# Kernel optimization log

Measured on AMD Instinct MI355X. Metric: run time of the kernel, lower is better.

The kernel has to match this reference:

```python
import jax, jax.numpy as jnp
import numpy as np
from jax import lax

N_NODES = 100000
N_EDGES = 1600000
NUM_GRAPHS = 2000
F_IN = 64
HIDDEN = 64
NUM_LAYERS = 3
K = 7
NUM_CLASSES = 10


def setup_inputs() -> dict:
    key = jax.random.key(0)
    ks = jax.random.split(key, 16)
    x = jax.random.normal(ks[0], (N_NODES, F_IN), jnp.float32)
    edge_index = jax.random.randint(ks[1], (2, N_EDGES), 0, N_NODES)
    batch = jnp.sort(jax.random.randint(ks[2], (N_NODES,), 0, NUM_GRAPHS))
    s = 1.0 / np.sqrt(HIDDEN)
    p = lambda k_, sh: jax.random.uniform(k_, sh, jnp.float32, -s, s)
    return dict(
        x=x, edge_index=edge_index, batch=batch,
        W1l=p(ks[3], (F_IN, HIDDEN)), b1=p(ks[4], (HIDDEN,)), W1r=p(ks[5], (F_IN, HIDDEN)),
        W2l=p(ks[6], (HIDDEN, HIDDEN)), b2=p(ks[7], (HIDDEN,)), W2r=p(ks[8], (HIDDEN, HIDDEN)),
        W3l=p(ks[9], (HIDDEN, HIDDEN)), b3=p(ks[10], (HIDDEN,)), W3r=p(ks[11], (HIDDEN, HIDDEN)),
        conv1d_w=p(ks[12], (32, HIDDEN, NUM_LAYERS)), conv1d_b=jnp.zeros((32,), jnp.float32),
        lin1_w=p(ks[13], (32 * (K - NUM_LAYERS + 1), HIDDEN)), lin1_b=jnp.zeros((HIDDEN,), jnp.float32),
        lin2_w=p(ks[14], (HIDDEN, NUM_CLASSES)), lin2_b=jnp.zeros((NUM_CLASSES,), jnp.float32),
    )


def _sage(x, src, dst, Wl, b, Wr):
    # PyG SAGEConv (aggr='mean'): lin_l(mean_j x_j) + lin_r(x_i); lin_l carries the bias.
    n = x.shape[0]
    msum = jax.ops.segment_sum(x[src], dst, num_segments=n)          # [N, D] gather+scatter
    cnt = jax.ops.segment_sum(jnp.ones((src.shape[0],), x.dtype), dst, num_segments=n)
    mean = msum / jnp.maximum(cnt, 1.0)[:, None]
    return mean @ Wl + b + x @ Wr


def _sort_pool(x, batch, num_graphs, k):
    # SortAggregation: per graph, sort nodes descending by last feature channel,
    # keep top-k, zero-pad short graphs, flatten to [B, k*D].
    N, D = x.shape
    perm = jnp.lexsort((-x[:, -1], batch))  # primary: graph id, secondary: desc last channel
    sb = batch[perm]
    counts = jax.ops.segment_sum(jnp.ones((N,), jnp.int32), batch, num_segments=num_graphs)
    starts = jnp.concatenate([jnp.zeros((1,), jnp.int32), jnp.cumsum(counts)[:-1]])
    rank = jnp.arange(N, dtype=jnp.int32) - starts[sb]
    valid = rank < k
    b_idx = jnp.where(valid, sb, num_graphs)  # route overflow nodes to dummy row
    r_idx = jnp.where(valid, rank, 0)
    out = jnp.zeros((num_graphs + 1, k, D), x.dtype).at[b_idx, r_idx].set(x[perm])
    return out[:num_graphs].reshape(num_graphs, k * D)


def reference(x, edge_index, batch, W1l, b1, W1r, W2l, b2, W2r, W3l, b3, W3r,
              conv1d_w, conv1d_b, lin1_w, lin1_b, lin2_w, lin2_b):
    src, dst = edge_index[0], edge_index[1]
    h = jax.nn.relu(_sage(x, src, dst, W1l, b1, W1r))
    h = jax.nn.relu(_sage(h, src, dst, W2l, b2, W2r))
    h = jax.nn.relu(_sage(h, src, dst, W3l, b3, W3r))
    g = _sort_pool(h, batch, NUM_GRAPHS, K)                       # [B, K*H]
    g = g.reshape(NUM_GRAPHS, K, HIDDEN).transpose(0, 2, 1)       # [B, H, K]
    c = lax.conv_general_dilated(g, conv1d_w, (1,), 'VALID',
                                 dimension_numbers=('NCH', 'OIH', 'NCH'))
    c = jax.nn.relu(c + conv1d_b[None, :, None])                  # [B, 32, K-ks+1]
    flat = c.reshape(NUM_GRAPHS, -1)
    h1 = jax.nn.relu(flat @ lin1_w + lin1_b)                      # dropout = identity (eval)
    logits = h1 @ lin2_w + lin2_b
    return jax.nn.log_softmax(logits, axis=-1)
```

## Files before the change

kernel.cpp:

```cpp
#include <hip/hip_runtime.h>
#include <hip/hip_bf16.h>

#define NN 100000
#define NE 1600000
#define NG 2000
#define KTOP 7

#define BNODES 128
#define NBKT 782
#define EPB 8192
#define NL1B 196
#define L2CAP 4096

#define GEMM_BLOCKS 768
#define SMEM_FLOATS (64 * 68 + 2 * 64 * 64)

#define FMA4C(av, B, acc) do { \
    acc[0] = fmaf(av, B.x, acc[0]); acc[1] = fmaf(av, B.y, acc[1]); \
    acc[2] = fmaf(av, B.z, acc[2]); acc[3] = fmaf(av, B.w, acc[3]); } while (0)

__device__ __forceinline__ void gemm_body(int bid, int nblocks, float* smem,
        const float* __restrict__ X, const float* __restrict__ Wl,
        const float* __restrict__ Wr, const float* __restrict__ bias,
        float* __restrict__ XL, float* __restrict__ T, int n) {
    float* As = smem;
    float* Bl = smem + 64 * 68;
    float* Br = Bl + 64 * 64;
    int t = threadIdx.x;

    #pragma unroll
    for (int q = 0; q < 4; ++q) {
        int idx = t + q * 256;
        ((float4*)Bl)[idx] = ((const float4*)Wl)[idx];
        ((float4*)Br)[idx] = ((const float4*)Wr)[idx];
    }
    int ty4 = (t >> 4) * 4, tx4 = (t & 15) * 4;
    float b0 = bias[tx4 + 0], b1v = bias[tx4 + 1], b2v = bias[tx4 + 2], b3v = bias[tx4 + 3];
    int ntiles = (n + 63) / 64;
    for (int tile = bid; tile < ntiles; tile += nblocks) {
        int n0 = tile * 64;
        #pragma unroll
        for (int q = 0; q < 4; ++q) {
            int f = t + q * 256;
            int node = f >> 4, seg = f & 15;
            int g = n0 + node;
            float4 v = make_float4(0.f, 0.f, 0.f, 0.f);
            if (g < n) v = *(const float4*)&X[(size_t)g * 64 + seg * 4];
            *(float4*)&As[node * 68 + seg * 4] = v;
        }
        __syncthreads();
        float accl[4][4] = {{0.f}}, accr[4][4] = {{0.f}};
        for (int kc = 0; kc < 64; kc += 4) {
            float4 Av[4], L[4], R[4];
            #pragma unroll
            for (int i = 0; i < 4; ++i) Av[i] = *(const float4*)&As[(ty4 + i) * 68 + kc];
            #pragma unroll
            for (int j = 0; j < 4; ++j) {
                L[j] = *(const float4*)&Bl[(kc + j) * 64 + tx4];
                R[j] = *(const float4*)&Br[(kc + j) * 64 + tx4];
            }
            #pragma unroll
            for (int i = 0; i < 4; ++i) {
                FMA4C(Av[i].x, L[0], accl[i]); FMA4C(Av[i].y, L[1], accl[i]);
                FMA4C(Av[i].z, L[2], accl[i]); FMA4C(Av[i].w, L[3], accl[i]);
                FMA4C(Av[i].x, R[0], accr[i]); FMA4C(Av[i].y, R[1], accr[i]);
                FMA4C(Av[i].z, R[2], accr[i]); FMA4C(Av[i].w, R[3], accr[i]);
            }
        }
        #pragma unroll
        for (int i = 0; i < 4; ++i) {
            int g = n0 + ty4 + i;
            if (g < n) {
                *(float4*)&XL[(size_t)g * 64 + tx4] =
                    make_float4(accl[i][0], accl[i][1], accl[i][2], accl[i][3]);
                *(float4*)&T[(size_t)g * 64 + tx4] =
                    make_float4(accr[i][0] + b0, accr[i][1] + b1v, accr[i][2] + b2v, accr[i][3] + b3v);
            }
        }
        __syncthreads();
    }
}

__global__ __launch_bounds__(256) void k_gemm(const float* __restrict__ X,
        const float* __restrict__ Wl, const float* __restrict__ Wr,
        const float* __restrict__ bias,
        float* __restrict__ XL, float* __restrict__ T, int n) {
    __shared__ float smem[SMEM_FLOATS];
    gemm_body(blockIdx.x, GEMM_BLOCKS, smem, X, Wl, Wr, bias, XL, T, n);
}

__global__ __launch_bounds__(256) void k_front(const float* __restrict__ X,
        const float* __restrict__ Wl, const float* __restrict__ Wr,
        const float* __restrict__ bias, float* __restrict__ XL, float* __restrict__ T,
        const int* __restrict__ edst, int* __restrict__ bh,
        const int* __restrict__ bat, int* __restrict__ gstart) {
    __shared__ float smem[SMEM_FLOATS];
    int bid = blockIdx.x, t = threadIdx.x;
    if (bid < GEMM_BLOCKS) {
        gemm_body(bid, GEMM_BLOCKS, smem, X, Wl, Wr, bias, XL, T, NN);
    } else if (bid < GEMM_BLOCKS + NL1B) {
        int bk = bid - GEMM_BLOCKS;
        int* h = (int*)smem;
        for (int q = t; q < NBKT; q += 256) h[q] = 0;
        __syncthreads();
        int e0 = bk * EPB, e1 = min(e0 + EPB, NE);
        for (int e = e0 + t; e < e1; e += 256) atomicAdd(&h[edst[e] >> 7], 1);
        __syncthreads();
        for (int q = t; q < NBKT; q += 256) bh[bk * NBKT + q] = h[q];
    } else {
        int g = (bid - GEMM_BLOCKS - NL1B) * 256 + t;
        if (g <= NG) {
            int lo = 0, hi = NN;
            while (lo < hi) { int mid = (lo + hi) >> 1; if (bat[mid] < g) lo = mid + 1; else hi = mid; }
            gstart[g] = lo;
        }
    }
}

__global__ void k_colscan(int* __restrict__ bh, int* __restrict__ btot) {
    __shared__ int carry;
    int b = blockIdx.x, t = threadIdx.x;
    if (t == 0) carry = 0;
    __syncthreads();
    for (int base = 0; base < NL1B; base += 64) {
        int idx = base + t;
        int v = (idx < NL1B) ? bh[idx * NBKT + b] : 0;
        int x = v;
        #pragma unroll
        for (int off = 1; off < 64; off <<= 1) {
            int y = __shfl_up(x, off);
            if (t >= off) x += y;
        }
        int c = carry;
        if (idx < NL1B) bh[idx * NBKT + b] = c + x - v;
        __syncthreads();
        if (t == 63) carry = c + x;
        __syncthreads();
    }
    if (t == 0) btot[b] = carry;
}

__global__ void k_btscan(const int* __restrict__ btot, int* __restrict__ bstart) {
    __shared__ int s[1024];
    int t = threadIdx.x;
    int v = (t < NBKT) ? btot[t] : 0;
    s[t] = v; __syncthreads();
    for (int off = 1; off < 1024; off <<= 1) {
        int y = (t >= off) ? s[t - off] : 0;
        __syncthreads();
        s[t] += y;
        __syncthreads();
    }
    if (t < NBKT) bstart[t] = s[t] - v;
    if (t == NBKT - 1) bstart[NBKT] = s[t];
}

__global__ __launch_bounds__(256) void k_bscatter(const int* __restrict__ esrc,
        const int* __restrict__ edst, const int* __restrict__ bh,
        const int* __restrict__ bstart, int* __restrict__ ebuf) {
    __shared__ int cur[NBKT];
    int t = threadIdx.x, bk = blockIdx.x;
    for (int q = t; q < NBKT; q += 256) cur[q] = bstart[q] + bh[bk * NBKT + q];
    __syncthreads();
    int e0 = bk * EPB, e1 = min(e0 + EPB, NE);
    for (int e = e0 + t; e < e1; e += 256) {
        int d = edst[e], s = esrc[e];
        int pos = atomicAdd(&cur[d >> 7], 1);
        ebuf[pos] = s | ((d & 127) << 20);
    }
}

__global__ __launch_bounds__(128) void k_bbuild(const int* __restrict__ ebuf,
        const int* __restrict__ bstart, int* __restrict__ ce, int* __restrict__ ptr) {
    __shared__ int lord[L2CAP];
    __shared__ int cnt[BNODES], sc[BNODES], cursor[BNODES];
    int b = blockIdx.x, t = threadIdx.x;
    int base = bstart[b], nb = bstart[b + 1] - base;
    cnt[t] = 0;
    __syncthreads();
    for (int j = t; j < nb; j += 128) atomicAdd(&cnt[ebuf[base + j] >> 20], 1);
    __syncthreads();
    int v = cnt[t]; sc[t] = v; __syncthreads();
    for (int off = 1; off < 128; off <<= 1) {
        int y = (t >= off) ? sc[t - off] : 0;
        __syncthreads();
        sc[t] += y;
        __syncthreads();
    }
    int segend = sc[t], segstart = sc[t] - v;
    cursor[t] = segstart;
    __syncthreads();
    bool fits = (nb <= L2CAP);
    for (int j = t; j < nb; j += 128) {
        int pv = ebuf[base + j];
        int node = pv >> 20;
        int pos = atomicAdd(&cursor[node], 1);
        if (fits) lord[pos] = pv & 0xFFFFF;
        else ce[base + pos] = pv & 0xFFFFF;
    }
    __syncthreads();
    if (fits) {
        for (int a = segstart + 1; a < segend; ++a) {
            int val = lord[a]; int j = a - 1;
            while (j >= segstart && lord[j] > val) { lord[j + 1] = lord[j]; --j; }
            lord[j + 1] = val;
        }
        __syncthreads();
        for (int j = t; j < nb; j += 128) ce[base + j] = lord[j];
    } else {
        for (int a = segstart + 1; a < segend; ++a) {
            int val = ce[base + a]; int j = a - 1;
            while (j >= segstart && ce[base + j] > val) { ce[base + j + 1] = ce[base + j]; --j; }
            ce[base + j + 1] = val;
        }
    }
    int node = b * BNODES + t;
    if (node <= NN) ptr[node] = base + segstart;
}

__global__ __launch_bounds__(256) void k_aggregate(const float* __restrict__ XL,
        float* __restrict__ Hout, const int* __restrict__ ptr, const int* __restrict__ ce,
        int n, float* __restrict__ key) {
    int wave = threadIdx.x >> 6, lane = threadIdx.x & 63;
    int i = blockIdx.x * 4 + wave;
    if (i >= n) return;
    int s = ptr[i], e = ptr[i + 1];
    int g = lane >> 4;
    int c4 = (lane & 15) * 4;
    float4 tv = *(const float4*)&Hout[(size_t)i * 64 + c4];
    float4 acc = make_float4(0.f, 0.f, 0.f, 0.f);
    int a = s;
    for (; a + 16 <= e; a += 16) {
        int r0 = ce[a + g], r1 = ce[a + 4 + g], r2 = ce[a + 8 + g], r3 = ce[a + 12 + g];
        float4 v0 = *(const float4*)&XL[(size_t)r0 * 64 + c4];
        float4 v1 = *(const float4*)&XL[(size_t)r1 * 64 + c4];
        float4 v2 = *(const float4*)&XL[(size_t)r2 * 64 + c4];
        float4 v3 = *(const float4*)&XL[(size_t)r3 * 64 + c4];
        acc.x += (v0.x + v1.x) + (v2.x + v3.x);
        acc.y += (v0.y + v1.y) + (v2.y + v3.y);
        acc.z += (v0.z + v1.z) + (v2.z + v3.z);
        acc.w += (v0.w + v1.w) + (v2.w + v3.w);
    }
    for (; a + 4 <= e; a += 4) {
        int r0 = ce[a + g];
        float4 v0 = *(const float4*)&XL[(size_t)r0 * 64 + c4];
        acc.x += v0.x; acc.y += v0.y; acc.z += v0.z; acc.w += v0.w;
    }
    if (g < e - a) {
        int r0 = ce[a + g];
        float4 v0 = *(const float4*)&XL[(size_t)r0 * 64 + c4];
        acc.x += v0.x; acc.y += v0.y; acc.z += v0.z; acc.w += v0.w;
    }
    #pragma unroll
    for (int off = 16; off < 64; off <<= 1) {
        acc.x += __shfl_xor(acc.x, off);
        acc.y += __shfl_xor(acc.y, off);
        acc.z += __shfl_xor(acc.z, off);
        acc.w += __shfl_xor(acc.w, off);
    }
    if (g == 0) {
        float cm = fmaxf((float)(e - s), 1.f);
        float4 h;
        h.x = fmaxf(acc.x / cm + tv.x, 0.f);
        h.y = fmaxf(acc.y / cm + tv.y, 0.f);
        h.z = fmaxf(acc.z / cm + tv.z, 0.f);
        h.w = fmaxf(acc.w / cm + tv.w, 0.f);
        *(float4*)&Hout[(size_t)i * 64 + c4] = h;
        if (key && (lane & 15) == 15) key[i] = h.w;
    }
}

__global__ __launch_bounds__(256) void k_topk(const float* __restrict__ key,
        const int* __restrict__ gstart, int* __restrict__ idx7, int G) {
    int wv = threadIdx.x >> 6, lane = threadIdx.x & 63;
    int b = blockIdx.x * 4 + wv;
    if (b >= G) return;
    int s = gstart[b], e = gstart[b + 1];
    float pk = 3.4e38f; int pi = -1;
    for (int r = 0; r < KTOP; ++r) {
        float bk = -1.f; int bi = -1;
        for (int i = s + lane; i < e; i += 64) {
            float k = key[i];
            bool elig = (k < pk) || (k == pk && i > pi);
            if (elig && (k > bk || (k == bk && (unsigned)i < (unsigned)bi))) { bk = k; bi = i; }
        }
        #pragma unroll
        for (int off = 1; off < 64; off <<= 1) {
            float ok = __shfl_xor(bk, off);
            int   oi = __shfl_xor(bi, off);
            if (ok > bk || (ok == bk && (unsigned)oi < (unsigned)bi)) { bk = ok; bi = oi; }
        }
        if (lane == 0) idx7[b * KTOP + r] = bi;
        pk = bk; pi = bi;
    }
}

__global__ __launch_bounds__(256) void k_head(const float* __restrict__ h3,
        const int* __restrict__ idx7,
        const float* __restrict__ cw, const float* __restrict__ cb,
        const float* __restrict__ l1w, const float* __restrict__ l1b,
        const float* __restrict__ l2w, const float* __restrict__ l2b,
        float* __restrict__ out, int G) {
    __shared__ float sw[32 * 64 * 3];
    __shared__ float s2w[64 * 10];
    __shared__ float sg[4][KTOP][64];
    __shared__ float sflat[4][160];
    __shared__ float sh1[4][64];
    __shared__ float slog[4][10];
    int t = threadIdx.x;
    for (int q = t; q < 32 * 64 * 3; q += 256) sw[q] = cw[q];
    for (int q = t; q < 640; q += 256) s2w[q] = l2w[q];
    int wv = t >> 6, lane = t & 63;
    int b = blockIdx.x * 4 + wv;
    for (int r = 0; r < KTOP; ++r) {
        int idx = idx7[b * KTOP + r];
        sg[wv][r][lane] = (idx >= 0) ? h3[(size_t)idx * 64 + lane] : 0.f;
    }
    __syncthreads();
    for (int idx = lane; idx < 160; idx += 64) {
        int o = idx / 5, p = idx % 5;
        float acc = cb[o];
        #pragma unroll
        for (int dt = 0; dt < 3; ++dt) {
            const float* wrow = &sw[(o * 64) * 3 + dt];
            const float* grow = &sg[wv][p + dt][0];
            for (int i = 0; i < 64; ++i) acc = fmaf(wrow[i * 3], grow[i], acc);
        }
        sflat[wv][idx] = fmaxf(acc, 0.f);
    }
    __syncthreads();
    {
        float acc = l1b[lane];
        for (int k = 0; k < 160; ++k) acc = fmaf(sflat[wv][k], l1w[k * 64 + lane], acc);
        sh1[wv][lane] = fmaxf(acc, 0.f);
    }
    __syncthreads();
    if (lane < 10) {
        float acc = l2b[lane];
        for (int k = 0; k < 64; ++k) acc = fmaf(sh1[wv][k], s2w[k * 10 + lane], acc);
        slog[wv][lane] = acc;
    }
    __syncthreads();
    if (lane < 10) {
        float m = -3.4e38f;
        for (int j = 0; j < 10; ++j) m = fmaxf(m, slog[wv][j]);
        float ssum = 0.f;
        for (int j = 0; j < 10; ++j) ssum += expf(slog[wv][j] - m);
        out[b * 10 + lane] = slog[wv][lane] - m - logf(ssum);
    }
}

extern "C" void kernel_launch(void* const* d_in, const int* in_sizes, int n_in,
                              void* d_out, int out_size, void* d_ws, size_t ws_size,
                              hipStream_t stream) {
    const float* x   = (const float*)d_in[0];
    const int*   ei  = (const int*)d_in[1];
    const int*   bat = (const int*)d_in[2];
    const float* W1l = (const float*)d_in[3], *b1 = (const float*)d_in[4], *W1r = (const float*)d_in[5];
    const float* W2l = (const float*)d_in[6], *b2 = (const float*)d_in[7], *W2r = (const float*)d_in[8];
    const float* W3l = (const float*)d_in[9], *b3 = (const float*)d_in[10], *W3r = (const float*)d_in[11];
    const float* cw  = (const float*)d_in[12], *cb  = (const float*)d_in[13];
    const float* l1w = (const float*)d_in[14], *l1b = (const float*)d_in[15];
    const float* l2w = (const float*)d_in[16], *l2b = (const float*)d_in[17];
    float* out = (float*)d_out;
    const int* esrc = ei;
    const int* edst = ei + NE;

    char* w = (char*)d_ws;
    size_t off = 0;
    auto take = [&](size_t bytes) { void* p = w + off; off = (off + bytes + 255) & ~(size_t)255; return p; };
    int*   bh      = (int*)take((size_t)NL1B * NBKT * 4);
    int*   btot    = (int*)take((size_t)NBKT * 4);
    int*   bstart  = (int*)take((size_t)(NBKT + 1) * 4);
    int*   gstart  = (int*)take((size_t)(NG + 1) * 4);
    int*   idx7    = (int*)take((size_t)NG * KTOP * 4);
    int*   ebuf    = (int*)take((size_t)NE * 4);
    int*   csr_ptr = (int*)take((size_t)(NN + 1) * 4);
    int*   csr_e   = (int*)take((size_t)NE * 4);
    float* XL      = (float*)take((size_t)NN * 64 * 4);
    float* Ha      = (float*)take((size_t)NN * 64 * 4);
    float* Hb      = (float*)take((size_t)NN * 64 * 4);
    float* key     = (float*)take((size_t)NN * 4);

    k_front<<<GEMM_BLOCKS + NL1B + 8, 256, 0, stream>>>(x, W1l, W1r, b1, XL, Ha,
                                                        edst, bh, bat, gstart);
    k_colscan<<<NBKT, 64, 0, stream>>>(bh, btot);
    k_btscan <<<1, 1024, 0, stream>>>(btot, bstart);
    k_bscatter<<<NL1B, 256, 0, stream>>>(esrc, edst, bh, bstart, ebuf);
    k_bbuild <<<NBKT, 128, 0, stream>>>(ebuf, bstart, csr_e, csr_ptr);

    k_aggregate<<<(NN + 3) / 4, 256, 0, stream>>>(XL, Ha, csr_ptr, csr_e, NN, nullptr);
    k_gemm<<<GEMM_BLOCKS, 256, 0, stream>>>(Ha, W2l, W2r, b2, XL, Hb, NN);
    k_aggregate<<<(NN + 3) / 4, 256, 0, stream>>>(XL, Hb, csr_ptr, csr_e, NN, nullptr);
    k_gemm<<<GEMM_BLOCKS, 256, 0, stream>>>(Hb, W3l, W3r, b3, XL, Ha, NN);
    k_aggregate<<<(NN + 3) / 4, 256, 0, stream>>>(XL, Ha, csr_ptr, csr_e, NN, key);

    k_topk<<<(NG + 3) / 4, 256, 0, stream>>>(key, gstart, idx7, NG);
    k_head<<<NG / 4, 256, 0, stream>>>(Ha, idx7, cw, cb, l1w, l1b, l2w, l2b, out, NG);
}
```

Baseline: 375.8 us.

## Fuse neighbor aggregation into next-layer GEMM and merge top-k into head

Each layer's mean aggregation and ReLU are now computed straight into the shared-memory A tile of the next layer's dual GEMM, so the hidden activation is never written to or re-read from global memory. The aggregation mapping also changes from one wave per node (16 lanes per float4 column group, with shuffle reductions) to four threads per node, each accumulating 16 contiguous features. The top-k selection is folded into the head kernel, and the idx7 buffer plus two launches are removed. The trade-off is less memory-level parallelism per node in the gather and fewer edges in flight per wave, which could hurt latency hiding. T is updated in place within a tile, and each tile reads its own T rows before any thread writes them.

```diff
diff --git a/kernel.cpp b/kernel.cpp
--- a/kernel.cpp
+++ b/kernel.cpp
@@ -13,31 +13,89 @@
 #define L2CAP 4096
 
 #define GEMM_BLOCKS 768
+#define NTILES 1563
 #define SMEM_FLOATS (64 * 68 + 2 * 64 * 64)
+
+#define ACC4(A, V) do { A.x += V.x; A.y += V.y; A.z += V.z; A.w += V.w; } while (0)
+#define ACC4P(A, U, W) do { A.x += U.x + W.x; A.y += U.y + W.y; \
+                            A.z += U.z + W.z; A.w += U.w + W.w; } while (0)
+
+__device__ __forceinline__ void agg_node(const float* __restrict__ XLp, const int* __restrict__ ce,
+        int s, int e, int fo, float4& a0, float4& a1, float4& a2, float4& a3) {
+    int a = s;
+    for (; a + 2 <= e; a += 2) {
+        const float4* p0 = (const float4*)(XLp + ((size_t)ce[a] << 6) + fo);
+        const float4* p1 = (const float4*)(XLp + ((size_t)ce[a + 1] << 6) + fo);
+        float4 u0 = p0[0], u1 = p0[1], u2 = p0[2], u3 = p0[3];
+        float4 w0 = p1[0], w1 = p1[1], w2 = p1[2], w3 = p1[3];
+        ACC4P(a0, u0, w0); ACC4P(a1, u1, w1); ACC4P(a2, u2, w2); ACC4P(a3, u3, w3);
+    }
+    if (a < e) {
+        const float4* p0 = (const float4*)(XLp + ((size_t)ce[a] << 6) + fo);
+        float4 u0 = p0[0], u1 = p0[1], u2 = p0[2], u3 = p0[3];
+        ACC4(a0, u0); ACC4(a1, u1); ACC4(a2, u2); ACC4(a3, u3);
+    }
+}
 
 #define FMA4C(av, B, acc) do { \
     acc[0] = fmaf(av, B.x, acc[0]); acc[1] = fmaf(av, B.y, acc[1]); \
     acc[2] = fmaf(av, B.z, acc[2]); acc[3] = fmaf(av, B.w, acc[3]); } while (0)
 
-__device__ __forceinline__ void gemm_body(int bid, int nblocks, float* smem,
-        const float* __restrict__ X, const float* __restrict__ Wl,
-        const float* __restrict__ Wr, const float* __restrict__ bias,
-        float* __restrict__ XL, float* __restrict__ T, int n) {
-    float* As = smem;
-    float* Bl = smem + 64 * 68;
-    float* Br = Bl + 64 * 64;
-    int t = threadIdx.x;
-
+__device__ __forceinline__ void gemm_tile(float* As, float* Bl, float* Br,
+        int n0, int ty4, int tx4, float b0, float b1v, float b2v, float b3v,
+        float* __restrict__ XL, float* __restrict__ T) {
+    float accl[4][4] = {{0.f}}, accr[4][4] = {{0.f}};
+    for (int kc = 0; kc < 64; kc += 4) {
+        float4 Av[4], L[4], R[4];
+        #pragma unroll
+        for (int i = 0; i < 4; ++i) Av[i] = *(const float4*)&As[(ty4 + i) * 68 + kc];
+        #pragma unroll
+        for (int j = 0; j < 4; ++j) {
+            L[j] = *(const float4*)&Bl[(kc + j) * 64 + tx4];
+            R[j] = *(const float4*)&Br[(kc + j) * 64 + tx4];
+        }
+        #pragma unroll
+        for (int i = 0; i < 4; ++i) {
+            FMA4C(Av[i].x, L[0], accl[i]); FMA4C(Av[i].y, L[1], accl[i]);
+            FMA4C(Av[i].z, L[2], accl[i]); FMA4C(Av[i].w, L[3], accl[i]);
+            FMA4C(Av[i].x, R[0], accr[i]); FMA4C(Av[i].y, R[1], accr[i]);
+            FMA4C(Av[i].z, R[2], accr[i]); FMA4C(Av[i].w, R[3], accr[i]);
+        }
+    }
+    #pragma unroll
+    for (int i = 0; i < 4; ++i) {
+        int g = n0 + ty4 + i;
+        if (g < NN) {
+            *(float4*)&XL[(size_t)g * 64 + tx4] =
+                make_float4(accl[i][0], accl[i][1], accl[i][2], accl[i][3]);
+            *(float4*)&T[(size_t)g * 64 + tx4] =
+                make_float4(accr[i][0] + b0, accr[i][1] + b1v, accr[i][2] + b2v, accr[i][3] + b3v);
+        }
+    }
+}
+
+__device__ __forceinline__ void stage_weights(float* Bl, float* Br,
+        const float* __restrict__ Wl, const float* __restrict__ Wr, int t) {
     #pragma unroll
     for (int q = 0; q < 4; ++q) {
         int idx = t + q * 256;
         ((float4*)Bl)[idx] = ((const float4*)Wl)[idx];
         ((float4*)Br)[idx] = ((const float4*)Wr)[idx];
     }
+}
+
+__device__ __forceinline__ void gemm_body(int bid, int nblocks, float* smem,
+        const float* __restrict__ X, const float* __restrict__ Wl,
+        const float* __restrict__ Wr, const float* __restrict__ bias,
+        float* __restrict__ XL, float* __restrict__ T) {
+    float* As = smem;
+    float* Bl = smem + 64 * 68;
+    float* Br = Bl + 64 * 64;
+    int t = threadIdx.x;
+    stage_weights(Bl, Br, Wl, Wr, t);
     int ty4 = (t >> 4) * 4, tx4 = (t & 15) * 4;
     float b0 = bias[tx4 + 0], b1v = bias[tx4 + 1], b2v = bias[tx4 + 2], b3v = bias[tx4 + 3];
-    int ntiles = (n + 63) / 64;
-    for (int tile = bid; tile < ntiles; tile += nblocks) {
+    for (int tile = bid; tile < NTILES; tile += nblocks) {
         int n0 = tile * 64;
         #pragma unroll
         for (int q = 0; q < 4; ++q) {
@@ -45,48 +103,80 @@
             int node = f >> 4, seg = f & 15;
             int g = n0 + node;
             float4 v = make_float4(0.f, 0.f, 0.f, 0.f);
-            if (g < n) v = *(const float4*)&X[(size_t)g * 64 + seg * 4];
+            if (g < NN) v = *(const float4*)&X[(size_t)g * 64 + seg * 4];
             *(float4*)&As[node * 68 + seg * 4] = v;
         }
         __syncthreads();
-        float accl[4][4] = {{0.f}}, accr[4][4] = {{0.f}};
-        for (int kc = 0; kc < 64; kc += 4) {
-            float4 Av[4], L[4], R[4];
-            #pragma unroll
-            for (int i = 0; i < 4; ++i) Av[i] = *(const float4*)&As[(ty4 + i) * 68 + kc];
-            #pragma unroll
-            for (int j = 0; j < 4; ++j) {
-                L[j] = *(const float4*)&Bl[(kc + j) * 64 + tx4];
-                R[j] = *(const float4*)&Br[(kc + j) * 64 + tx4];
-            }
-            #pragma unroll
-            for (int i = 0; i < 4; ++i) {
-                FMA4C(Av[i].x, L[0], accl[i]); FMA4C(Av[i].y, L[1], accl[i]);
-                FMA4C(Av[i].z, L[2], accl[i]); FMA4C(Av[i].w, L[3], accl[i]);
-                FMA4C(Av[i].x, R[0], accr[i]); FMA4C(Av[i].y, R[1], accr[i]);
-                FMA4C(Av[i].z, R[2], accr[i]); FMA4C(Av[i].w, R[3], accr[i]);
-            }
-        }
-        #pragma unroll
-        for (int i = 0; i < 4; ++i) {
-            int g = n0 + ty4 + i;
-            if (g < n) {
-                *(float4*)&XL[(size_t)g * 64 + tx4] =
-                    make_float4(accl[i][0], accl[i][1], accl[i][2], accl[i][3]);
-                *(float4*)&T[(size_t)g * 64 + tx4] =
-                    make_float4(accr[i][0] + b0, accr[i][1] + b1v, accr[i][2] + b2v, accr[i][3] + b3v);
-            }
-        }
-        __syncthreads();
-    }
-}
-
-__global__ __launch_bounds__(256) void k_gemm(const float* __restrict__ X,
+        gemm_tile(As, Bl, Br, n0, ty4, tx4, b0, b1v, b2v, b3v, XL, T);
+        __syncthreads();
+    }
+}
+
+__global__ __launch_bounds__(256) void k_aggemm(const float* __restrict__ XL_in,
+        float* __restrict__ T, const int* __restrict__ ptr, const int* __restrict__ ce,
         const float* __restrict__ Wl, const float* __restrict__ Wr,
-        const float* __restrict__ bias,
-        float* __restrict__ XL, float* __restrict__ T, int n) {
+        const float* __restrict__ bias, float* __restrict__ XL_out) {
     __shared__ float smem[SMEM_FLOATS];
-    gemm_body(blockIdx.x, GEMM_BLOCKS, smem, X, Wl, Wr, bias, XL, T, n);
+    float* As = smem;
+    float* Bl = smem + 64 * 68;
+    float* Br = Bl + 64 * 64;
+    int t = threadIdx.x;
+    stage_weights(Bl, Br, Wl, Wr, t);
+    int node_l = t >> 2;
+    int fo = (t & 3) * 16;
+    int ty4 = (t >> 4) * 4, tx4 = (t & 15) * 4;
+    float b0 = bias[tx4 + 0], b1v = bias[tx4 + 1], b2v = bias[tx4 + 2], b3v = bias[tx4 + 3];
+    for (int tile = blockIdx.x; tile < NTILES; tile += GEMM_BLOCKS) {
+        int n0 = tile * 64;
+        int i = n0 + node_l;
+        float4 h0 = make_float4(0.f, 0.f, 0.f, 0.f), h1 = h0, h2 = h0, h3 = h0;
+        if (i < NN) {
+            int s = ptr[i], e = ptr[i + 1];
+            agg_node(XL_in, ce, s, e, fo, h0, h1, h2, h3);
+            float inv = 1.f / fmaxf((float)(e - s), 1.f);
+            const float4* tp = (const float4*)(T + ((size_t)i << 6) + fo);
+            float4 t0 = tp[0], t1 = tp[1], t2 = tp[2], t3 = tp[3];
+            h0.x = fmaxf(h0.x * inv + t0.x, 0.f); h0.y = fmaxf(h0.y * inv + t0.y, 0.f);
+            h0.z = fmaxf(h0.z * inv + t0.z, 0.f); h0.w = fmaxf(h0.w * inv + t0.w, 0.f);
+            h1.x = fmaxf(h1.x * inv + t1.x, 0.f); h1.y = fmaxf(h1.y * inv + t1.y, 0.f);
+            h1.z = fmaxf(h1.z * inv + t1.z, 0.f); h1.w = fmaxf(h1.w * inv + t1.w, 0.f);
+            h2.x = fmaxf(h2.x * inv + t2.x, 0.f); h2.y = fmaxf(h2.y * inv + t2.y, 0.f);
+            h2.z = fmaxf(h2.z * inv + t2.z, 0.f); h2.w = fmaxf(h2.w * inv + t2.w, 0.f);
+            h3.x = fmaxf(h3.x * inv + t3.x, 0.f); h3.y = fmaxf(h3.y * inv + t3.y, 0.f);
+            h3.z = fmaxf(h3.z * inv + t3.z, 0.f); h3.w = fmaxf(h3.w * inv + t3.w, 0.f);
+        }
+        float* dst = &As[node_l * 68 + fo];
+        ((float4*)dst)[0] = h0; ((float4*)dst)[1] = h1;
+        ((float4*)dst)[2] = h2; ((float4*)dst)[3] = h3;
+        __syncthreads();
+        gemm_tile(As, Bl, Br, n0, ty4, tx4, b0, b1v, b2v, b3v, XL_out, T);
+        __syncthreads();
+    }
+}
+
+__global__ __launch_bounds__(256) void k_agg3(const float* __restrict__ XL_in,
+        float* __restrict__ T, const int* __restrict__ ptr, const int* __restrict__ ce,
+        float* __restrict__ key) {
+    int t = threadIdx.x;
+    int i = blockIdx.x * 64 + (t >> 2);
+    int fo = (t & 3) * 16;
+    if (i >= NN) return;
+    int s = ptr[i], e = ptr[i + 1];
+    float4 h0 = make_float4(0.f, 0.f, 0.f, 0.f), h1 = h0, h2 = h0, h3 = h0;
+    agg_node(XL_in, ce, s, e, fo, h0, h1, h2, h3);
+    float inv = 1.f / fmaxf((float)(e - s), 1.f);
+    float4* tp = (float4*)(T + ((size_t)i << 6) + fo);
+    float4 t0 = tp[0], t1 = tp[1], t2 = tp[2], t3 = tp[3];
+    h0.x = fmaxf(h0.x * inv + t0.x, 0.f); h0.y = fmaxf(h0.y * inv + t0.y, 0.f);
+    h0.z = fmaxf(h0.z * inv + t0.z, 0.f); h0.w = fmaxf(h0.w * inv + t0.w, 0.f);
+    h1.x = fmaxf(h1.x * inv + t1.x, 0.f); h1.y = fmaxf(h1.y * inv + t1.y, 0.f);
+    h1.z = fmaxf(h1.z * inv + t1.z, 0.f); h1.w = fmaxf(h1.w * inv + t1.w, 0.f);
+    h2.x = fmaxf(h2.x * inv + t2.x, 0.f); h2.y = fmaxf(h2.y * inv + t2.y, 0.f);
+    h2.z = fmaxf(h2.z * inv + t2.z, 0.f); h2.w = fmaxf(h2.w * inv + t2.w, 0.f);
+    h3.x = fmaxf(h3.x * inv + t3.x, 0.f); h3.y = fmaxf(h3.y * inv + t3.y, 0.f);
+    h3.z = fmaxf(h3.z * inv + t3.z, 0.f); h3.w = fmaxf(h3.w * inv + t3.w, 0.f);
+    tp[0] = h0; tp[1] = h1; tp[2] = h2; tp[3] = h3;
+    if ((t & 3) == 3) key[i] = h3.w;
 }
 
 __global__ __launch_bounds__(256) void k_front(const float* __restrict__ X,
@@ -97,7 +187,7 @@
     __shared__ float smem[SMEM_FLOATS];
     int bid = blockIdx.x, t = threadIdx.x;
     if (bid < GEMM_BLOCKS) {
-        gemm_body(bid, GEMM_BLOCKS, smem, X, Wl, Wr, bias, XL, T, NN);
+        gemm_body(bid, GEMM_BLOCKS, smem, X, Wl, Wr, bias, XL, T);
     } else if (bid < GEMM_BLOCKS + NL1B) {
         int bk = bid - GEMM_BLOCKS;
         int* h = (int*)smem;
@@ -218,85 +308,8 @@
     if (node <= NN) ptr[node] = base + segstart;
 }
 
-__global__ __launch_bounds__(256) void k_aggregate(const float* __restrict__ XL,
-        float* __restrict__ Hout, const int* __restrict__ ptr, const int* __restrict__ ce,
-        int n, float* __restrict__ key) {
-    int wave = threadIdx.x >> 6, lane = threadIdx.x & 63;
-    int i = blockIdx.x * 4 + wave;
-    if (i >= n) return;
-    int s = ptr[i], e = ptr[i + 1];
-    int g = lane >> 4;
-    int c4 = (lane & 15) * 4;
-    float4 tv = *(const float4*)&Hout[(size_t)i * 64 + c4];
-    float4 acc = make_float4(0.f, 0.f, 0.f, 0.f);
-    int a = s;
-    for (; a + 16 <= e; a += 16) {
-        int r0 = ce[a + g], r1 = ce[a + 4 + g], r2 = ce[a + 8 + g], r3 = ce[a + 12 + g];
-        float4 v0 = *(const float4*)&XL[(size_t)r0 * 64 + c4];
-        float4 v1 = *(const float4*)&XL[(size_t)r1 * 64 + c4];
-        float4 v2 = *(const float4*)&XL[(size_t)r2 * 64 + c4];
-        float4 v3 = *(const float4*)&XL[(size_t)r3 * 64 + c4];
-        acc.x += (v0.x + v1.x) + (v2.x + v3.x);
-        acc.y += (v0.y + v1.y) + (v2.y + v3.y);
-        acc.z += (v0.z + v1.z) + (v2.z + v3.z);
-        acc.w += (v0.w + v1.w) + (v2.w + v3.w);
-    }
-    for (; a + 4 <= e; a += 4) {
-        int r0 = ce[a + g];
-        float4 v0 = *(const float4*)&XL[(size_t)r0 * 64 + c4];
-        acc.x += v0.x; acc.y += v0.y; acc.z += v0.z; acc.w += v0.w;
-    }
-    if (g < e - a) {
-        int r0 = ce[a + g];
-        float4 v0 = *(const float4*)&XL[(size_t)r0 * 64 + c4];
-        acc.x += v0.x; acc.y += v0.y; acc.z += v0.z; acc.w += v0.w;
-    }
-    #pragma unroll
-    for (int off = 16; off < 64; off <<= 1) {
-        acc.x += __shfl_xor(acc.x, off);
-        acc.y += __shfl_xor(acc.y, off);
-        acc.z += __shfl_xor(acc.z, off);
-        acc.w += __shfl_xor(acc.w, off);
-    }
-    if (g == 0) {
-        float cm = fmaxf((float)(e - s), 1.f);
-        float4 h;
-        h.x = fmaxf(acc.x / cm + tv.x, 0.f);
-        h.y = fmaxf(acc.y / cm + tv.y, 0.f);
-        h.z = fmaxf(acc.z / cm + tv.z, 0.f);
-        h.w = fmaxf(acc.w / cm + tv.w, 0.f);
-        *(float4*)&Hout[(size_t)i * 64 + c4] = h;
-        if (key && (lane & 15) == 15) key[i] = h.w;
-    }
-}
-
-__global__ __launch_bounds__(256) void k_topk(const float* __restrict__ key,
-        const int* __restrict__ gstart, int* __restrict__ idx7, int G) {
-    int wv = threadIdx.x >> 6, lane = threadIdx.x & 63;
-    int b = blockIdx.x * 4 + wv;
-    if (b >= G) return;
-    int s = gstart[b], e = gstart[b + 1];
-    float pk = 3.4e38f; int pi = -1;
-    for (int r = 0; r < KTOP; ++r) {
-        float bk = -1.f; int bi = -1;
-        for (int i = s + lane; i < e; i += 64) {
-            float k = key[i];
-            bool elig = (k < pk) || (k == pk && i > pi);
-            if (elig && (k > bk || (k == bk && (unsigned)i < (unsigned)bi))) { bk = k; bi = i; }
-        }
-        #pragma unroll
-        for (int off = 1; off < 64; off <<= 1) {
-            float ok = __shfl_xor(bk, off);
-            int   oi = __shfl_xor(bi, off);
-            if (ok > bk || (ok == bk && (unsigned)oi < (unsigned)bi)) { bk = ok; bi = oi; }
-        }
-        if (lane == 0) idx7[b * KTOP + r] = bi;
-        pk = bk; pi = bi;
-    }
-}
-
-__global__ __launch_bounds__(256) void k_head(const float* __restrict__ h3,
-        const int* __restrict__ idx7,
+__global__ __launch_bounds__(256) void k_tail(const float* __restrict__ key,
+        const int* __restrict__ gstart, const float* __restrict__ h3,
         const float* __restrict__ cw, const float* __restrict__ cb,
         const float* __restrict__ l1w, const float* __restrict__ l1b,
         const float* __restrict__ l2w, const float* __restrict__ l2b,
@@ -312,9 +325,25 @@
     for (int q = t; q < 640; q += 256) s2w[q] = l2w[q];
     int wv = t >> 6, lane = t & 63;
     int b = blockIdx.x * 4 + wv;
-    for (int r = 0; r < KTOP; ++r) {
-        int idx = idx7[b * KTOP + r];
-        sg[wv][r][lane] = (idx >= 0) ? h3[(size_t)idx * 64 + lane] : 0.f;
+    {
+        int s = gstart[b], e = gstart[b + 1];
+        float pk = 3.4e38f; int pi = -1;
+        for (int r = 0; r < KTOP; ++r) {
+            float bk = -1.f; int bi = -1;
+            for (int i = s + lane; i < e; i += 64) {
+                float k = key[i];
+                bool elig = (k < pk) || (k == pk && i > pi);
+                if (elig && (k > bk || (k == bk && (unsigned)i < (unsigned)bi))) { bk = k; bi = i; }
+            }
+            #pragma unroll
+            for (int off = 1; off < 64; off <<= 1) {
+                float ok = __shfl_xor(bk, off);
+                int   oi = __shfl_xor(bi, off);
+                if (ok > bk || (ok == bk && (unsigned)oi < (unsigned)bi)) { bk = ok; bi = oi; }
+            }
+            sg[wv][r][lane] = (bi >= 0) ? h3[(size_t)bi * 64 + lane] : 0.f;
+            pk = bk; pi = bi;
+        }
     }
     __syncthreads();
     for (int idx = lane; idx < 160; idx += 64) {
@@ -373,28 +402,24 @@
     int*   btot    = (int*)take((size_t)NBKT * 4);
     int*   bstart  = (int*)take((size_t)(NBKT + 1) * 4);
     int*   gstart  = (int*)take((size_t)(NG + 1) * 4);
-    int*   idx7    = (int*)take((size_t)NG * KTOP * 4);
     int*   ebuf    = (int*)take((size_t)NE * 4);
     int*   csr_ptr = (int*)take((size_t)(NN + 1) * 4);
     int*   csr_e   = (int*)take((size_t)NE * 4);
-    float* XL      = (float*)take((size_t)NN * 64 * 4);
-    float* Ha      = (float*)take((size_t)NN * 64 * 4);
-    float* Hb      = (float*)take((size_t)NN * 64 * 4);
+    float* XLa     = (float*)take((size_t)NN * 64 * 4);
+    float* XLb     = (float*)take((size_t)NN * 64 * 4);
+    float* T       = (float*)take((size_t)NN * 64 * 4);
     float* key     = (float*)take((size_t)NN * 4);
 
-    k_front<<<GEMM_BLOCKS + NL1B + 8, 256, 0, stream>>>(x, W1l, W1r, b1, XL, Ha,
+    k_front<<<GEMM_BLOCKS + NL1B + 8, 256, 0, stream>>>(x, W1l, W1r, b1, XLa, T,
                                                         edst, bh, bat, gstart);
     k_colscan<<<NBKT, 64, 0, stream>>>(bh, btot);
     k_btscan <<<1, 1024, 0, stream>>>(btot, bstart);
     k_bscatter<<<NL1B, 256, 0, stream>>>(esrc, edst, bh, bstart, ebuf);
     k_bbuild <<<NBKT, 128, 0, stream>>>(ebuf, bstart, csr_e, csr_ptr);
 
-    k_aggregate<<<(NN + 3) / 4, 256, 0, stream>>>(XL, Ha, csr_ptr, csr_e, NN, nullptr);
-    k_gemm<<<GEMM_BLOCKS, 256, 0, stream>>>(Ha, W2l, W2r, b2, XL, Hb, NN);
-    k_aggregate<<<(NN + 3) / 4, 256, 0, stream>>>(XL, Hb, csr_ptr, csr_e, NN, nullptr);
-    k_gemm<<<GEMM_BLOCKS, 256, 0, stream>>>(Hb, W3l, W3r, b3, XL, Ha, NN);
-    k_aggregate<<<(NN + 3) / 4, 256, 0, stream>>>(XL, Ha, csr_ptr, csr_e, NN, key);
-
-    k_topk<<<(NG + 3) / 4, 256, 0, stream>>>(key, gstart, idx7, NG);
-    k_head<<<NG / 4, 256, 0, stream>>>(Ha, idx7, cw, cb, l1w, l1b, l2w, l2b, out, NG);
-}
+    k_aggemm<<<GEMM_BLOCKS, 256, 0, stream>>>(XLa, T, csr_ptr, csr_e, W2l, W2r, b2, XLb);
+    k_aggemm<<<GEMM_BLOCKS, 256, 0, stream>>>(XLb, T, csr_ptr, csr_e, W3l, W3r, b3, XLa);
+    k_agg3<<<NTILES, 256, 0, stream>>>(XLa, T, csr_ptr, csr_e, key);
+
+    k_tail<<<NG / 4, 256, 0, stream>>>(key, gstart, T, cw, cb, l1w, l1b, l2w, l2b, out, NG);
+}
```

Measured after the change: 364.9 us. 1.03x faster.
